# Kernel optimization log

Measured on AMD Instinct MI355X. Metric: run time of the kernel, lower is better.

## Reference

```python
import jax, jax.numpy as jnp
import numpy as np

N_NODES = 50000
N_EDGES = 1600000
IN_FEATS = 128
HIDDEN = 16
HEADS = 8
SLOPE = 0.2


def setup_inputs() -> dict:
    key = jax.random.key(0)
    ks = jax.random.split(key, 9)
    feat = jax.random.normal(ks[0], (N_NODES, IN_FEATS), dtype=jnp.float32)
    edge_src = jax.random.randint(ks[1], (N_EDGES,), 0, N_NODES, dtype=jnp.int32)
    edge_dst = jax.random.randint(ks[2], (N_EDGES,), 0, N_NODES, dtype=jnp.int32)
    # layer 0: in=128 -> H*F=128 ; layer 1: in=128 (concat of layer 0) -> 128
    s0 = 1.0 / np.sqrt(IN_FEATS)
    W0 = jax.random.normal(ks[3], (IN_FEATS, HEADS * HIDDEN), dtype=jnp.float32) * s0
    al0 = jax.random.normal(ks[4], (HEADS, HIDDEN), dtype=jnp.float32) * 0.1
    ar0 = jax.random.normal(ks[5], (HEADS, HIDDEN), dtype=jnp.float32) * 0.1
    W1 = jax.random.normal(ks[6], (HEADS * HIDDEN, HEADS * HIDDEN), dtype=jnp.float32) * s0
    al1 = jax.random.normal(ks[7], (HEADS, HIDDEN), dtype=jnp.float32) * 0.1
    ar1 = jax.random.normal(ks[8], (HEADS, HIDDEN), dtype=jnp.float32) * 0.1
    return {"feat": feat, "edge_src": edge_src, "edge_dst": edge_dst,
            "W0": W0, "al0": al0, "ar0": ar0, "W1": W1, "al1": al1, "ar1": ar1}


def _gat_conv(feat, W, al, ar, src, dst):
    """One DGL-style GATConv: no bias, no residual, no dropout, no activation."""
    n = feat.shape[0]
    h = (feat @ W).reshape(n, HEADS, HIDDEN)              # [N,H,F]
    el = jnp.sum(h * al, axis=-1)                          # [N,H]
    er = jnp.sum(h * ar, axis=-1)                          # [N,H]
    e = jax.nn.leaky_relu(el[src] + er[dst], negative_slope=SLOPE)  # [E,H]
    # edge softmax over incoming edges of each dst node
    m = jax.ops.segment_max(e, dst, num_segments=n)        # [N,H]
    ex = jnp.exp(e - m[dst])                               # [E,H]
    denom = jax.ops.segment_sum(ex, dst, num_segments=n)   # [N,H]
    alpha = ex / jnp.where(denom[dst] > 0, denom[dst], 1.0)
    # message passing: gather src features, weight, scatter-add to dst
    out = jax.ops.segment_sum(h[src] * alpha[:, :, None], dst, num_segments=n)
    return out                                             # [N,H,F]


def reference(feat, edge_src, edge_dst, W0, al0, ar0, W1, al1, ar1):
    n = feat.shape[0]
    # step 1 + concat (flatten heads)
    x = _gat_conv(feat, W0, al0, ar0, edge_src, edge_dst).reshape(n, HEADS * HIDDEN)
    # step 2 + concat
    x = _gat_conv(x, W1, al1, ar1, edge_src, edge_dst).reshape(n, HEADS * HIDDEN)
    return x
```

## Files before the change

kernel.cpp:

```cpp
#include <hip/hip_runtime.h>
#include <hip/hip_bf16.h>


#define HEADS 8
#define HID 16
#define HF 128
#define SLOPE 0.2f

#define BSHIFT 8
#define BRANGE 256
#define CHUNK 4096

typedef __attribute__((ext_vector_type(8))) short bf16x8;
typedef __attribute__((ext_vector_type(4))) float f32x4;

static __device__ __forceinline__ unsigned int f2bf(float f) {
    unsigned int u = __float_as_uint(f);
    u += 0x7fffu + ((u >> 16) & 1u);
    return u >> 16;
}


template <bool XBF16>
static __device__ __forceinline__ void gemm_body(
    int blk, unsigned short* xs, unsigned short* ws,
    const void* __restrict__ Xv, const unsigned short* __restrict__ Wtb,
    const float* __restrict__ AL, const float* __restrict__ AR,
    unsigned short* __restrict__ Hb, float* __restrict__ EL,
    float* __restrict__ ER, int n) {
    int t = threadIdx.x;
    int row0 = blk * 64;

    {
        int r = t >> 2;
        int gr = row0 + r;
        unsigned int rowbase = r * 256;
        unsigned int sw = (r & 7) << 4;
        if (XBF16) {
            unsigned int kb0 = (t & 3) * 64;
            const char* src = (const char*)Xv + (size_t)gr * 256 + kb0;
            #pragma unroll
            for (int i = 0; i < 4; ++i) {
                int4 v = (gr < n) ? *(const int4*)(src + i * 16)
                                  : make_int4(0, 0, 0, 0);
                *(int4*)((char*)xs + rowbase + ((kb0 + i * 16) ^ sw)) = v;
            }
        } else {
            int k0 = (t & 3) * 32;
            float4 f[8];
            if (gr < n) {
                const float4* p = (const float4*)((const float*)Xv + (size_t)gr * HF + k0);
                #pragma unroll
                for (int i = 0; i < 8; ++i) f[i] = p[i];
            } else {
                #pragma unroll
                for (int i = 0; i < 8; ++i) f[i] = make_float4(0.f, 0.f, 0.f, 0.f);
            }
            #pragma unroll
            for (int g2 = 0; g2 < 4; ++g2) {
                float4 a = f[g2 * 2], b = f[g2 * 2 + 1];
                int4 pk;
                pk.x = (int)(f2bf(a.x) | (f2bf(a.y) << 16));
                pk.y = (int)(f2bf(a.z) | (f2bf(a.w) << 16));
                pk.z = (int)(f2bf(b.x) | (f2bf(b.y) << 16));
                pk.w = (int)(f2bf(b.z) | (f2bf(b.w) << 16));
                unsigned int addr = rowbase + ((unsigned)((k0 + g2 * 8) * 2) ^ sw);
                *(int4*)((char*)xs + addr) = pk;
            }
        }
    }
    {
        int c = t >> 1;
        unsigned int kb0 = (t & 1) * 128;
        const int4* src = (const int4*)((const char*)Wtb + (size_t)c * 256 + kb0);
        unsigned int sw = (c & 7) << 4;
        #pragma unroll
        for (int i = 0; i < 8; ++i) {
            int4 v = src[i];
            unsigned int addr = c * 256 + ((kb0 + i * 16) ^ sw);
            *(int4*)((char*)ws + addr) = v;
        }
    }
    __syncthreads();

    int wv = t >> 6;
    int l = t & 63;
    int lr = l & 15;
    int g = l >> 4;

    bf16x8 bfr[4];
    {
        int r = wv * 16 + lr;
        unsigned int rowbase = r * 256;
        unsigned int sw = (r & 7) << 4;
        #pragma unroll
        for (int s = 0; s < 4; ++s) {
            unsigned int kbyte = (unsigned)((s * 32 + g * 8) * 2);
            bfr[s] = *(bf16x8*)((char*)xs + rowbase + (kbyte ^ sw));
        }
    }

    f32x4 acc[8];
    #pragma unroll
    for (int ct = 0; ct < 8; ++ct) acc[ct] = (f32x4){0.f, 0.f, 0.f, 0.f};

    #pragma unroll
    for (int ct = 0; ct < 8; ++ct) {
        int c = ct * 16 + lr;
        unsigned int rowbase = c * 256;
        unsigned int sw = (c & 7) << 4;
        #pragma unroll
        for (int s = 0; s < 4; ++s) {
            unsigned int kbyte = (unsigned)((s * 32 + g * 8) * 2);
            bf16x8 af = *(bf16x8*)((char*)ws + rowbase + (kbyte ^ sw));
            acc[ct] = __builtin_amdgcn_mfma_f32_16x16x32_bf16(af, bfr[s], acc[ct], 0, 0, 0);
        }
    }

    int grow = row0 + wv * 16 + lr;
    bool valid = grow < n;

    if (valid) {
        #pragma unroll
        for (int ct = 0; ct < 8; ++ct) {
            ushort4 hb4 = make_ushort4(
                (unsigned short)f2bf(acc[ct][0]), (unsigned short)f2bf(acc[ct][1]),
                (unsigned short)f2bf(acc[ct][2]), (unsigned short)f2bf(acc[ct][3]));
            *(ushort4*)(Hb + (size_t)grow * HF + ct * 16 + g * 4) = hb4;
        }
    }

    #pragma unroll
    for (int ct = 0; ct < 8; ++ct) {
        float e1 = 0.f, e2 = 0.f;
        #pragma unroll
        for (int rg = 0; rg < 4; ++rg) {
            float alv = AL[ct * 16 + g * 4 + rg];
            float arv = AR[ct * 16 + g * 4 + rg];
            e1 += acc[ct][rg] * alv;
            e2 += acc[ct][rg] * arv;
        }
        e1 += __shfl_xor(e1, 16); e1 += __shfl_xor(e1, 32);
        e2 += __shfl_xor(e2, 16); e2 += __shfl_xor(e2, 32);
        if (g == 0 && valid) {
            EL[grow * HEADS + ct] = e1;
            ER[grow * HEADS + ct] = e2;
        }
    }
}


static __device__ __forceinline__ void wtrans_body(
    int blk, const float* __restrict__ W, unsigned short* __restrict__ Wtb) {
    int gid = blk * 256 + threadIdx.x;
    int c = gid >> 3;
    int k0 = (gid & 7) * 16;
    #pragma unroll
    for (int q = 0; q < 4; ++q) {
        int k = k0 + q * 4;
        ushort4 o = make_ushort4(
            (unsigned short)f2bf(W[(k + 0) * HF + c]),
            (unsigned short)f2bf(W[(k + 1) * HF + c]),
            (unsigned short)f2bf(W[(k + 2) * HF + c]),
            (unsigned short)f2bf(W[(k + 3) * HF + c]));
        *(ushort4*)(Wtb + (size_t)c * HF + k) = o;
    }
}


__global__ __launch_bounds__(256) void fused0_kernel(
    const float* __restrict__ X, const unsigned short* __restrict__ Wtb0,
    const float* __restrict__ AL, const float* __restrict__ AR,
    unsigned short* __restrict__ Hb, float* __restrict__ EL,
    float* __restrict__ ER, int n, int gGemm,
    const int* __restrict__ edst, int* __restrict__ bhistT, int E, int nb, int nblk,
    const float* __restrict__ W1, unsigned short* __restrict__ wtb1) {
    __shared__ __align__(16) unsigned char lds[48 * 1024];
    int b = blockIdx.x;
    if (b < gGemm) {
        gemm_body<false>(b, (unsigned short*)lds, (unsigned short*)(lds + 16384),
                         X, Wtb0, AL, AR, Hb, EL, ER, n);
    } else if (b < gGemm + nblk) {
        int blk = b - gGemm;
        int* h = (int*)lds;
        int t = threadIdx.x;
        h[t] = 0;
        __syncthreads();
        int base = blk * CHUNK;
        int end = base + CHUNK; if (end > E) end = E;
        for (int i = base + t; i < end; i += 256)
            atomicAdd(&h[edst[i] >> BSHIFT], 1);
        __syncthreads();
        if (t < nb) bhistT[(size_t)t * nblk + blk] = h[t];
    } else {
        wtrans_body(b - gGemm - nblk, W1, wtb1);
    }
}


__global__ __launch_bounds__(256) void wtrans_kernel(const float* __restrict__ W,
                                                     unsigned short* __restrict__ Wtb) {
    wtrans_body(blockIdx.x, W, Wtb);
}

template <bool XBF16>
__global__ __launch_bounds__(256) void gemm_mfma_kernel(
    const void* __restrict__ Xv, const unsigned short* __restrict__ Wtb,
    const float* __restrict__ AL, const float* __restrict__ AR,
    unsigned short* __restrict__ Hb, float* __restrict__ EL,
    float* __restrict__ ER, int n) {
    __shared__ __align__(16) unsigned short xs[64 * HF];
    __shared__ __align__(16) unsigned short ws[HF * HF];
    gemm_body<XBF16>(blockIdx.x, xs, ws, Xv, Wtb, AL, AR, Hb, EL, ER, n);
}

__global__ __launch_bounds__(64) void bscan1_kernel(
    const int* __restrict__ bhistT, int* __restrict__ boffT,
    int* __restrict__ btot, int nblk) {
    int b = blockIdx.x;
    int l = threadIdx.x;
    int carry = 0;
    for (int c0 = 0; c0 < nblk; c0 += 64) {
        int blk = c0 + l;
        int v = (blk < nblk) ? bhistT[(size_t)b * nblk + blk] : 0;
        int x = v;
        #pragma unroll
        for (int off = 1; off < 64; off <<= 1) {
            int y = __shfl_up(x, off, 64);
            if (l >= off) x += y;
        }
        if (blk < nblk) boffT[(size_t)b * nblk + blk] = carry + x - v;
        carry += __shfl(x, 63);
    }
    if (l == 0) btot[b] = carry;
}

__global__ __launch_bounds__(256) void bscan2_kernel(
    const int* __restrict__ btot, int* __restrict__ bbase,
    int* __restrict__ rowptr, int nb, int N, int E) {
    __shared__ int s[256];
    int t = threadIdx.x;
    s[t] = (t < nb) ? btot[t] : 0;
    __syncthreads();
    #pragma unroll
    for (int off = 1; off < 256; off <<= 1) {
        int v = (t >= off) ? s[t - off] : 0;
        __syncthreads();
        s[t] += v;
        __syncthreads();
    }
    int excl = (t == 0) ? 0 : s[t - 1];
    if (t < nb) bbase[t] = excl;
    if (t == 0) { bbase[nb] = E; rowptr[N] = E; }
}

__global__ __launch_bounds__(512) void bucket_scatter_kernel(
    const int* __restrict__ src, const int* __restrict__ dst,
    const int* __restrict__ bhistT, const int* __restrict__ boffT,
    const int* __restrict__ bbase, int* __restrict__ stage,
    int E, int nb, int nblk) {
    __shared__ int lscan[BRANGE];
    __shared__ int lcur[BRANGE];
    __shared__ int gbase[BRANGE];
    __shared__ int sstage[CHUNK];
    int t = threadIdx.x;
    int blk = blockIdx.x;
    int base = blk * CHUNK;
    int end = base + CHUNK; if (end > E) end = E;

    if (t < 256) lscan[t] = (t < nb) ? bhistT[(size_t)t * nblk + blk] : 0;
    __syncthreads();
    #pragma unroll
    for (int off = 1; off < 256; off <<= 1) {
        int v = 0;
        if (t < 256 && t >= off) v = lscan[t - off];
        __syncthreads();
        if (t < 256) lscan[t] += v;
        __syncthreads();
    }
    int ex = 0;
    if (t < 256) ex = (t == 0) ? 0 : lscan[t - 1];
    __syncthreads();
    if (t < 256) {
        lcur[t] = ex;
        lscan[t] = ex;
        if (t < nb) gbase[t] = bbase[t] + boffT[(size_t)t * nblk + blk];
    }
    __syncthreads();

    for (int i = base + t; i < end; i += 512) {
        int d = dst[i];
        int b = d >> BSHIFT;
        int pos = atomicAdd(&lcur[b], 1);
        sstage[pos] = (src[i] & 0xFFFF) | ((d & (BRANGE - 1)) << 16) | (b << 24);
    }
    __syncthreads();

    int total = end - base;
    for (int i = t; i < total; i += 512) {
        int p = sstage[i];
        int b = ((unsigned)p) >> 24;
        int gpos = gbase[b] + (i - lscan[b]);
        stage[gpos] = p;
    }
}

__global__ __launch_bounds__(512) void bucket_csr_kernel(
    const int* __restrict__ stage, const int* __restrict__ bbase,
    int* __restrict__ rowptr, unsigned short* __restrict__ col, int N, int nb) {
    __shared__ int hist[BRANGE];
    __shared__ int lscan[BRANGE];
    __shared__ int lcur[BRANGE];
    int b = blockIdx.x;
    int t = threadIdx.x;
    int e0 = bbase[b], e1 = bbase[b + 1];
    if (t < BRANGE) hist[t] = 0;
    __syncthreads();
    for (int i = e0 + t; i < e1; i += 512)
        atomicAdd(&hist[(stage[i] >> 16) & (BRANGE - 1)], 1);
    __syncthreads();
    if (t < 256) lscan[t] = hist[t];
    __syncthreads();
    #pragma unroll
    for (int off = 1; off < 256; off <<= 1) {
        int v = 0;
        if (t < 256 && t >= off) v = lscan[t - off];
        __syncthreads();
        if (t < 256) lscan[t] += v;
        __syncthreads();
    }
    if (t < 256) {
        int ex = (t == 0) ? 0 : lscan[t - 1];
        lcur[t] = ex;
        int node = (b << BSHIFT) + t;
        if (node < N) rowptr[node] = e0 + ex;
    }
    __syncthreads();
    for (int i = e0 + t; i < e1; i += 512) {
        int p = stage[i];
        int pos = e0 + atomicAdd(&lcur[(p >> 16) & (BRANGE - 1)], 1);
        col[pos] = (unsigned short)(p & 0xFFFF);
    }
}


template <bool OBF16>
__global__ __launch_bounds__(256) void gat_aggregate_kernel(
    const unsigned int* __restrict__ HbU,
    const float* __restrict__ EL, const float* __restrict__ ER,
    const int* __restrict__ rowptr, const unsigned short* __restrict__ col,
    void* __restrict__ OUT, int n) {
    int wid = (int)((blockIdx.x * blockDim.x + threadIdx.x) >> 6);
    if (wid >= n) return;
    int lane = threadIdx.x & 63;
    int s0 = rowptr[wid], s1 = rowptr[wid + 1];
    if (s1 == s0) {
        if (OBF16) ((unsigned int*)OUT)[(size_t)wid * 64 + lane] = 0u;
        else ((float2*)OUT)[(size_t)wid * 64 + lane] = make_float2(0.f, 0.f);
        return;
    }

    int h = lane & 7;
    int j = lane >> 3;
    int hC = lane >> 3;
    float er_h = ER[wid * HEADS + h];

    float accx = 0.f, accy = 0.f;
    float dpart = 0.f;

    for (int base = s0; base < s1; base += 8) {
        int i = base + j;
        int icl = i < s1 ? i : s1 - 1;
        int sj = (int)col[icl];
        float e = EL[sj * HEADS + h] + er_h;
        e = fmaxf(e, SLOPE * e);
        float w = __expf(e);
        if (i >= s1) w = 0.f;
        dpart += w;

        if (base + 8 <= s1) {
            #pragma unroll
            for (int jj = 0; jj < 8; ++jj) {
                float wC = __shfl(w, jj * 8 + hC);
                int s = __builtin_amdgcn_readlane(sj, jj * 8);
                unsigned int pv = HbU[(size_t)s * 64 + lane];
                accx += wC * __uint_as_float(pv << 16);
                accy += wC * __uint_as_float(pv & 0xffff0000u);
            }
        } else {
            int ne = s1 - base;
            for (int jj = 0; jj < ne; ++jj) {
                float wC = __shfl(w, jj * 8 + hC);
                int s = __builtin_amdgcn_readlane(sj, jj * 8);
                unsigned int pv = HbU[(size_t)s * 64 + lane];
                accx += wC * __uint_as_float(pv << 16);
                accy += wC * __uint_as_float(pv & 0xffff0000u);
            }
        }
    }

    dpart += __shfl_xor(dpart, 8);
    dpart += __shfl_xor(dpart, 16);
    dpart += __shfl_xor(dpart, 32);
    float rC = 1.f / __shfl(dpart, hC);

    if (OBF16) {
        unsigned int o = f2bf(accx * rC) | (f2bf(accy * rC) << 16);
        ((unsigned int*)OUT)[(size_t)wid * 64 + lane] = o;
    } else {
        ((float2*)OUT)[(size_t)wid * 64 + lane] = make_float2(accx * rC, accy * rC);
    }
}


extern "C" void kernel_launch(void* const* d_in, const int* in_sizes, int n_in,
                              void* d_out, int out_size, void* d_ws, size_t ws_size,
                              hipStream_t stream) {
    const float* feat = (const float*)d_in[0];
    const int*   esrc = (const int*)d_in[1];
    const int*   edst = (const int*)d_in[2];
    const float* W0   = (const float*)d_in[3];
    const float* al0  = (const float*)d_in[4];
    const float* ar0  = (const float*)d_in[5];
    const float* W1   = (const float*)d_in[6];
    const float* al1  = (const float*)d_in[7];
    const float* ar1  = (const float*)d_in[8];
    float* out = (float*)d_out;

    const int N = in_sizes[0] / HF;
    const int E = in_sizes[1];
    const int nb = (N + BRANGE - 1) >> BSHIFT;
    const int nblk = (E + CHUNK - 1) / CHUNK;

    char* w = (char*)d_ws;
    auto alloc = [&](size_t bytes) -> void* {
        void* p = (void*)w;
        w += (bytes + 255) & ~(size_t)255;
        return p;
    };
    unsigned short* hb   = (unsigned short*)alloc((size_t)N * HF * 2);
    unsigned short* x1b  = (unsigned short*)alloc((size_t)N * HF * 2);
    float* el_buf = (float*)alloc((size_t)N * HEADS * 4);
    float* er_buf = (float*)alloc((size_t)N * HEADS * 4);
    int*   rowptr = (int*)alloc((size_t)(N + 1) * 4);
    unsigned short* col = (unsigned short*)alloc((size_t)E * 2);
    int*   bhistT = (int*)alloc((size_t)nb * nblk * 4);
    int*   boffT  = (int*)alloc((size_t)nb * nblk * 4);
    int*   btot   = (int*)alloc((size_t)nb * 4);
    int*   bbase  = (int*)alloc((size_t)(nb + 1) * 4);
    unsigned short* wtb0 = (unsigned short*)alloc((size_t)HF * HF * 2);
    unsigned short* wtb1 = (unsigned short*)alloc((size_t)HF * HF * 2);
    int*   stage  = (int*)alloc((size_t)E * 4);

    int gGemm = (N + 63) / 64;
    int gAgg  = (N * 64 + 255) / 256;

    wtrans_kernel<<<4, 256, 0, stream>>>(W0, wtb0);

    fused0_kernel<<<gGemm + nblk + 4, 256, 0, stream>>>(
        feat, wtb0, al0, ar0, hb, el_buf, er_buf, N, gGemm,
        edst, bhistT, E, nb, nblk, W1, wtb1);

    bscan1_kernel<<<nb, 64, 0, stream>>>(bhistT, boffT, btot, nblk);
    bscan2_kernel<<<1, 256, 0, stream>>>(btot, bbase, rowptr, nb, N, E);
    bucket_scatter_kernel<<<nblk, 512, 0, stream>>>(esrc, edst, bhistT, boffT,
                                                    bbase, stage, E, nb, nblk);
    bucket_csr_kernel<<<nb, 512, 0, stream>>>(stage, bbase, rowptr, col, N, nb);

    gat_aggregate_kernel<true><<<gAgg, 256, 0, stream>>>(
        (const unsigned int*)hb, el_buf, er_buf, rowptr, col, x1b, N);

    gemm_mfma_kernel<true><<<gGemm, 256, 0, stream>>>(x1b, wtb1, al1, ar1,
                                                      hb, el_buf, er_buf, N);
    gat_aggregate_kernel<false><<<gAgg, 256, 0, stream>>>(
        (const unsigned int*)hb, el_buf, er_buf, rowptr, col, out, N);
}
```

Before: 215.3 us.

## Restructure CSR build and layer-0 GEMM into fewer fused launches

```diff
diff --git a/kernel.cpp b/kernel.cpp
--- a/kernel.cpp
+++ b/kernel.cpp
@@ -168,50 +168,76 @@
 }
 
 
-__global__ __launch_bounds__(256) void fused0_kernel(
-    const float* __restrict__ X, const unsigned short* __restrict__ Wtb0,
-    const float* __restrict__ AL, const float* __restrict__ AR,
-    unsigned short* __restrict__ Hb, float* __restrict__ EL,
-    float* __restrict__ ER, int n, int gGemm,
+static __device__ __forceinline__ void csr_body(
+    int b, char* ldsc, const int* __restrict__ stage, const int* __restrict__ btot,
+    int* __restrict__ rowptr, unsigned short* __restrict__ col,
+    int N, int nb, int E) {
+    int* hist  = (int*)ldsc;
+    int* lscan = hist + 256;
+    int* lcur  = lscan + 256;
+    int* sb    = lcur + 256;
+    int t = threadIdx.x;
+    sb[t] = (t < nb) ? btot[t] : 0;
+    hist[t] = 0;
+    __syncthreads();
+    #pragma unroll
+    for (int off = 1; off < 256; off <<= 1) {
+        int v = (t >= off) ? sb[t - off] : 0;
+        __syncthreads();
+        sb[t] += v;
+        __syncthreads();
+    }
+    int e0 = (b == 0) ? 0 : sb[b - 1];
+    int e1 = sb[b];
+    if (b == 0 && t == 0) rowptr[N] = E;
+
+    for (int i = e0 + t; i < e1; i += 256)
+        atomicAdd(&hist[(stage[i] >> 16) & (BRANGE - 1)], 1);
+    __syncthreads();
+    lscan[t] = hist[t];
+    __syncthreads();
+    #pragma unroll
+    for (int off = 1; off < 256; off <<= 1) {
+        int v = (t >= off) ? lscan[t - off] : 0;
+        __syncthreads();
+        lscan[t] += v;
+        __syncthreads();
+    }
+    int ex = (t == 0) ? 0 : lscan[t - 1];
+    __syncthreads();
+    lcur[t] = ex;
+    int node = (b << BSHIFT) + t;
+    if (node < N) rowptr[node] = e0 + ex;
+    __syncthreads();
+    for (int i = e0 + t; i < e1; i += 256) {
+        int p = stage[i];
+        int pos = e0 + atomicAdd(&lcur[(p >> 16) & (BRANGE - 1)], 1);
+        col[pos] = (unsigned short)(p & 0xFFFF);
+    }
+}
+
+
+__global__ __launch_bounds__(256) void fused_pre_kernel(
     const int* __restrict__ edst, int* __restrict__ bhistT, int E, int nb, int nblk,
+    const float* __restrict__ W0, unsigned short* __restrict__ wtb0,
     const float* __restrict__ W1, unsigned short* __restrict__ wtb1) {
-    __shared__ __align__(16) unsigned char lds[48 * 1024];
+    __shared__ int h[BRANGE];
     int b = blockIdx.x;
-    if (b < gGemm) {
-        gemm_body<false>(b, (unsigned short*)lds, (unsigned short*)(lds + 16384),
-                         X, Wtb0, AL, AR, Hb, EL, ER, n);
-    } else if (b < gGemm + nblk) {
-        int blk = b - gGemm;
-        int* h = (int*)lds;
-        int t = threadIdx.x;
+    int t = threadIdx.x;
+    if (b < nblk) {
         h[t] = 0;
         __syncthreads();
-        int base = blk * CHUNK;
+        int base = b * CHUNK;
         int end = base + CHUNK; if (end > E) end = E;
         for (int i = base + t; i < end; i += 256)
             atomicAdd(&h[edst[i] >> BSHIFT], 1);
         __syncthreads();
-        if (t < nb) bhistT[(size_t)t * nblk + blk] = h[t];
+        if (t < nb) bhistT[(size_t)t * nblk + b] = h[t];
+    } else if (b < nblk + 4) {
+        wtrans_body(b - nblk, W0, wtb0);
     } else {
-        wtrans_body(b - gGemm - nblk, W1, wtb1);
-    }
-}
-
-
-__global__ __launch_bounds__(256) void wtrans_kernel(const float* __restrict__ W,
-                                                     unsigned short* __restrict__ Wtb) {
-    wtrans_body(blockIdx.x, W, Wtb);
-}
-
-template <bool XBF16>
-__global__ __launch_bounds__(256) void gemm_mfma_kernel(
-    const void* __restrict__ Xv, const unsigned short* __restrict__ Wtb,
-    const float* __restrict__ AL, const float* __restrict__ AR,
-    unsigned short* __restrict__ Hb, float* __restrict__ EL,
-    float* __restrict__ ER, int n) {
-    __shared__ __align__(16) unsigned short xs[64 * HF];
-    __shared__ __align__(16) unsigned short ws[HF * HF];
-    gemm_body<XBF16>(blockIdx.x, xs, ws, Xv, Wtb, AL, AR, Hb, EL, ER, n);
+        wtrans_body(b - nblk - 4, W1, wtb1);
+    }
 }
 
 __global__ __launch_bounds__(64) void bscan1_kernel(
@@ -235,47 +261,32 @@
     if (l == 0) btot[b] = carry;
 }
 
-__global__ __launch_bounds__(256) void bscan2_kernel(
-    const int* __restrict__ btot, int* __restrict__ bbase,
-    int* __restrict__ rowptr, int nb, int N, int E) {
-    __shared__ int s[256];
-    int t = threadIdx.x;
-    s[t] = (t < nb) ? btot[t] : 0;
-    __syncthreads();
-    #pragma unroll
-    for (int off = 1; off < 256; off <<= 1) {
-        int v = (t >= off) ? s[t - off] : 0;
-        __syncthreads();
-        s[t] += v;
-        __syncthreads();
-    }
-    int excl = (t == 0) ? 0 : s[t - 1];
-    if (t < nb) bbase[t] = excl;
-    if (t == 0) { bbase[nb] = E; rowptr[N] = E; }
-}
-
 __global__ __launch_bounds__(512) void bucket_scatter_kernel(
     const int* __restrict__ src, const int* __restrict__ dst,
     const int* __restrict__ bhistT, const int* __restrict__ boffT,
-    const int* __restrict__ bbase, int* __restrict__ stage,
+    const int* __restrict__ btot, int* __restrict__ stage,
     int E, int nb, int nblk) {
     __shared__ int lscan[BRANGE];
     __shared__ int lcur[BRANGE];
     __shared__ int gbase[BRANGE];
+    __shared__ int sb[BRANGE];
     __shared__ int sstage[CHUNK];
     int t = threadIdx.x;
     int blk = blockIdx.x;
     int base = blk * CHUNK;
     int end = base + CHUNK; if (end > E) end = E;
 
-    if (t < 256) lscan[t] = (t < nb) ? bhistT[(size_t)t * nblk + blk] : 0;
+    if (t < 256) {
+        lscan[t] = (t < nb) ? bhistT[(size_t)t * nblk + blk] : 0;
+        sb[t] = (t < nb) ? btot[t] : 0;
+    }
     __syncthreads();
     #pragma unroll
     for (int off = 1; off < 256; off <<= 1) {
-        int v = 0;
-        if (t < 256 && t >= off) v = lscan[t - off];
-        __syncthreads();
-        if (t < 256) lscan[t] += v;
+        int v = 0, u = 0;
+        if (t < 256 && t >= off) { v = lscan[t - off]; u = sb[t - off]; }
+        __syncthreads();
+        if (t < 256) { lscan[t] += v; sb[t] += u; }
         __syncthreads();
     }
     int ex = 0;
@@ -284,7 +295,10 @@
     if (t < 256) {
         lcur[t] = ex;
         lscan[t] = ex;
-        if (t < nb) gbase[t] = bbase[t] + boffT[(size_t)t * nblk + blk];
+        if (t < nb) {
+            int bb = (t == 0) ? 0 : sb[t - 1];
+            gbase[t] = bb + boffT[(size_t)t * nblk + blk];
+        }
     }
     __syncthreads();
 
@@ -305,42 +319,36 @@
     }
 }
 
-__global__ __launch_bounds__(512) void bucket_csr_kernel(
-    const int* __restrict__ stage, const int* __restrict__ bbase,
-    int* __restrict__ rowptr, unsigned short* __restrict__ col, int N, int nb) {
-    __shared__ int hist[BRANGE];
-    __shared__ int lscan[BRANGE];
-    __shared__ int lcur[BRANGE];
+
+__global__ __launch_bounds__(256) void fused_mid_kernel(
+    const int* __restrict__ stage, const int* __restrict__ btot,
+    int* __restrict__ rowptr, unsigned short* __restrict__ col,
+    int N, int nb, int E, int nCsr,
+    const float* __restrict__ X, const unsigned short* __restrict__ wtb0,
+    const float* __restrict__ AL, const float* __restrict__ AR,
+    unsigned short* __restrict__ Hb, float* __restrict__ EL,
+    float* __restrict__ ER) {
+    __shared__ __align__(16) unsigned char lds[48 * 1024];
     int b = blockIdx.x;
-    int t = threadIdx.x;
-    int e0 = bbase[b], e1 = bbase[b + 1];
-    if (t < BRANGE) hist[t] = 0;
-    __syncthreads();
-    for (int i = e0 + t; i < e1; i += 512)
-        atomicAdd(&hist[(stage[i] >> 16) & (BRANGE - 1)], 1);
-    __syncthreads();
-    if (t < 256) lscan[t] = hist[t];
-    __syncthreads();
-    #pragma unroll
-    for (int off = 1; off < 256; off <<= 1) {
-        int v = 0;
-        if (t < 256 && t >= off) v = lscan[t - off];
-        __syncthreads();
-        if (t < 256) lscan[t] += v;
-        __syncthreads();
-    }
-    if (t < 256) {
-        int ex = (t == 0) ? 0 : lscan[t - 1];
-        lcur[t] = ex;
-        int node = (b << BSHIFT) + t;
-        if (node < N) rowptr[node] = e0 + ex;
-    }
-    __syncthreads();
-    for (int i = e0 + t; i < e1; i += 512) {
-        int p = stage[i];
-        int pos = e0 + atomicAdd(&lcur[(p >> 16) & (BRANGE - 1)], 1);
-        col[pos] = (unsigned short)(p & 0xFFFF);
-    }
+    if (b < nCsr) {
+        csr_body(b, (char*)lds, stage, btot, rowptr, col, N, nb, E);
+    } else {
+        gemm_body<false>(b - nCsr, (unsigned short*)lds,
+                         (unsigned short*)(lds + 16384),
+                         X, wtb0, AL, AR, Hb, EL, ER, N);
+    }
+}
+
+
+template <bool XBF16>
+__global__ __launch_bounds__(256) void gemm_mfma_kernel(
+    const void* __restrict__ Xv, const unsigned short* __restrict__ Wtb,
+    const float* __restrict__ AL, const float* __restrict__ AR,
+    unsigned short* __restrict__ Hb, float* __restrict__ EL,
+    float* __restrict__ ER, int n) {
+    __shared__ __align__(16) unsigned short xs[64 * HF];
+    __shared__ __align__(16) unsigned short ws[HF * HF];
+    gemm_body<XBF16>(blockIdx.x, xs, ws, Xv, Wtb, AL, AR, Hb, EL, ER, n);
 }
 
 
@@ -447,7 +455,6 @@
     int*   bhistT = (int*)alloc((size_t)nb * nblk * 4);
     int*   boffT  = (int*)alloc((size_t)nb * nblk * 4);
     int*   btot   = (int*)alloc((size_t)nb * 4);
-    int*   bbase  = (int*)alloc((size_t)(nb + 1) * 4);
     unsigned short* wtb0 = (unsigned short*)alloc((size_t)HF * HF * 2);
     unsigned short* wtb1 = (unsigned short*)alloc((size_t)HF * HF * 2);
     int*   stage  = (int*)alloc((size_t)E * 4);
@@ -455,17 +462,14 @@
     int gGemm = (N + 63) / 64;
     int gAgg  = (N * 64 + 255) / 256;
 
-    wtrans_kernel<<<4, 256, 0, stream>>>(W0, wtb0);
-
-    fused0_kernel<<<gGemm + nblk + 4, 256, 0, stream>>>(
-        feat, wtb0, al0, ar0, hb, el_buf, er_buf, N, gGemm,
-        edst, bhistT, E, nb, nblk, W1, wtb1);
-
+    fused_pre_kernel<<<nblk + 8, 256, 0, stream>>>(edst, bhistT, E, nb, nblk,
+                                                   W0, wtb0, W1, wtb1);
     bscan1_kernel<<<nb, 64, 0, stream>>>(bhistT, boffT, btot, nblk);
-    bscan2_kernel<<<1, 256, 0, stream>>>(btot, bbase, rowptr, nb, N, E);
     bucket_scatter_kernel<<<nblk, 512, 0, stream>>>(esrc, edst, bhistT, boffT,
-                                                    bbase, stage, E, nb, nblk);
-    bucket_csr_kernel<<<nb, 512, 0, stream>>>(stage, bbase, rowptr, col, N, nb);
+                                                    btot, stage, E, nb, nblk);
+    fused_mid_kernel<<<nb + gGemm, 256, 0, stream>>>(
+        stage, btot, rowptr, col, N, nb, E, nb,
+        feat, wtb0, al0, ar0, hb, el_buf, er_buf);
 
     gat_aggregate_kernel<true><<<gAgg, 256, 0, stream>>>(
         (const unsigned int*)hb, el_buf, er_buf, rowptr, col, x1b, N);
```

Measured after the change: 211.3 us (median of 2 runs). About the same (-1.9%).
